# Performance work log

Hardware: AMD Instinct MI355X
Metric: run time of the kernel (lower is better)

## Reference

```python
import jax, jax.numpy as jnp
import numpy as np

D_E = 128
D_R = 128  # must equal D_E for the original torch code to typecheck
BN_EPS = 1e-5


def setup_inputs() -> dict:
    key = jax.random.key(0)
    ks = jax.random.split(key, 8)
    B, S = 16, 2048
    h = jax.random.normal(ks[0], (B, S, D_E), dtype=jnp.float32)
    r = jax.random.normal(ks[1], (B, S, D_R), dtype=jnp.float32)
    t = jax.random.normal(ks[2], (B, S, D_E), dtype=jnp.float32)
    # Xavier-uniform core tensor W: (d_r, d_e, d_e)
    limit = float(np.sqrt(6.0 / (D_R + D_E * D_E)))
    W = jax.random.uniform(ks[3], (D_R, D_E, D_E), minval=-limit, maxval=limit, dtype=jnp.float32)
    # BatchNorm1d params/buffers (inference mode)
    gamma0 = jnp.ones((D_E,), jnp.float32)
    beta0 = jnp.zeros((D_E,), jnp.float32)
    mean0 = 0.1 * jax.random.normal(ks[4], (D_E,), dtype=jnp.float32)
    var0 = jnp.abs(1.0 + 0.1 * jax.random.normal(ks[5], (D_E,), dtype=jnp.float32))
    gamma1 = jnp.ones((D_E,), jnp.float32)
    beta1 = jnp.zeros((D_E,), jnp.float32)
    mean1 = 0.1 * jax.random.normal(ks[6], (D_E,), dtype=jnp.float32)
    var1 = jnp.abs(1.0 + 0.1 * jax.random.normal(ks[7], (D_E,), dtype=jnp.float32))
    return {"h": h, "r": r, "t": t, "W": W,
            "gamma0": gamma0, "beta0": beta0, "mean0": mean0, "var0": var0,
            "gamma1": gamma1, "beta1": beta1, "mean1": mean1, "var1": var1}


def reference(h, r, t, W, gamma0, beta0, mean0, var0, gamma1, beta1, mean1, var1):
    B, S, D = h.shape  # D == d_e == d_r
    N = B * S
    # BatchNorm1d in eval mode over last dim; dropout is identity in eval.
    h_bn = (h - mean0) * jax.lax.rsqrt(var0 + BN_EPS) * gamma0 + beta0
    t_bn = (t - mean1) * jax.lax.rsqrt(var1 + BN_EPS) * gamma1 + beta1
    r2 = r.reshape(N, D)
    # torch.matmul((N,d_r), (d_r,d_e,d_e)) broadcasts -> shape (d_r, N, d_e):
    #   out[k, n, j] = sum_i r2[n, i] * W[k, i, j]
    # followed by .view(N, d_e, d_e) which reinterprets the flat buffer.
    W_mat = jnp.einsum('ni,kij->knj', r2, W).reshape(N, D, D)  # (N, d_e, d_e) after scrambled view
    # hr[n, j] = sum_d h_bn[n, d] * W_mat[n, d, j]
    hr = jnp.einsum('nd,ndj->nj', h_bn.reshape(N, D), W_mat)
    scores = jnp.sum(hr * t_bn.reshape(N, D), axis=-1)  # (N,)
    return scores.reshape(B, S)
```

## Files before the change

kernel.cpp:

```cpp
#include <hip/hip_runtime.h>


typedef __attribute__((ext_vector_type(8))) short bf16x8;
typedef __attribute__((ext_vector_type(4))) short s16x4;
typedef __attribute__((ext_vector_type(4))) float f32x4;

#define DPAD 136
#define BN_EPS 1e-5f

__device__ inline unsigned short f2bf(float f) {
  unsigned u = __builtin_bit_cast(unsigned, f);
  u += 0x7FFFu + ((u >> 16) & 1u);
  return (unsigned short)(u >> 16);
}
__device__ inline float bf2f(unsigned short h) {
  unsigned u = ((unsigned)h) << 16;
  return __builtin_bit_cast(float, u);
}
__device__ inline unsigned pack2bf(float lo, float hi) {
  return (unsigned)f2bf(lo) | ((unsigned)f2bf(hi) << 16);
}
__device__ inline bf16x8 cvt8(f32x4 lo, f32x4 hi) {
  bf16x8 o;
  o[0] = (short)f2bf(lo[0]); o[1] = (short)f2bf(lo[1]);
  o[2] = (short)f2bf(lo[2]); o[3] = (short)f2bf(lo[3]);
  o[4] = (short)f2bf(hi[0]); o[5] = (short)f2bf(hi[1]);
  o[6] = (short)f2bf(hi[2]); o[7] = (short)f2bf(hi[3]);
  return o;
}

__device__ inline int xcd_map(int bid) { return (bid & 7) * 64 + (bid >> 3); }

__global__ __launch_bounds__(256, 3) void k_A(
    const float* __restrict__ t, const float* __restrict__ W,
    const float* __restrict__ gamma1, const float* __restrict__ beta1,
    const float* __restrict__ mean1, const float* __restrict__ var1,
    unsigned short* __restrict__ V) {
  __shared__ short LW[128 * DPAD];
  const int tid = threadIdx.x;
  const int c = tid & 31;
  const int rr = tid >> 5;
  const int wv_ = tid >> 6;
  const int lane = tid & 63;
  const int l16 = lane & 15;
  const int quad = lane >> 4;

  const int wg = xcd_map(blockIdx.x);
  const int k = wg >> 2;
  const int quarter = wg & 3;
  const int nrow = k * 256 + quarter * 64 + wv_ * 16 + l16;

  const float* tp = t + (size_t)nrow * 128;
  bf16x8 tf[4];
#pragma unroll
  for (int ks = 0; ks < 4; ++ks) {
    const int K0 = ks * 32 + quad * 8;
    f32x4 g0 = *(const f32x4*)(gamma1 + K0), g1 = *(const f32x4*)(gamma1 + K0 + 4);
    f32x4 b0 = *(const f32x4*)(beta1  + K0), b1 = *(const f32x4*)(beta1  + K0 + 4);
    f32x4 m0 = *(const f32x4*)(mean1  + K0), m1 = *(const f32x4*)(mean1  + K0 + 4);
    f32x4 v0 = *(const f32x4*)(var1   + K0), v1 = *(const f32x4*)(var1   + K0 + 4);
    f32x4 t0 = *(const f32x4*)(tp + K0),     t1 = *(const f32x4*)(tp + K0 + 4);
    f32x4 lo, hi;
    for (int q = 0; q < 4; ++q) {
      const float s0 = g0[q] * rsqrtf(v0[q] + BN_EPS);
      lo[q] = t0[q] * s0 + (b0[q] - m0[q] * s0);
      const float s1 = g1[q] * rsqrtf(v1[q] + BN_EPS);
      hi[q] = t1[q] * s1 + (b1[q] - m1[q] * s1);
    }
    tf[ks] = cvt8(lo, hi);
  }

  const float* wbase = W + (size_t)k * 16384;
#pragma unroll
  for (int it = 0; it < 16; ++it) {
    const int m = it * 8 + rr;
    f32x4 wvv = *(const f32x4*)(wbase + m * 128 + c * 4);
    s16x4 wb;
    for (int q = 0; q < 4; ++q) wb[q] = (short)f2bf(wvv[q]);
    *(s16x4*)(&LW[m * DPAD + c * 4]) = wb;
  }
  __syncthreads();

  f32x4 acc[8];
#pragma unroll
  for (int nt = 0; nt < 8; ++nt) acc[nt] = (f32x4){0.f, 0.f, 0.f, 0.f};

  __builtin_amdgcn_s_setprio(1);
#pragma unroll
  for (int ks = 0; ks < 4; ++ks) {
    const int K0 = ks * 32 + quad * 8;
    bf16x8 b[8];
#pragma unroll
    for (int nt = 0; nt < 8; ++nt)
      b[nt] = *(const bf16x8*)(&LW[(nt * 16 + l16) * DPAD + K0]);
#pragma unroll
    for (int nt = 0; nt < 8; ++nt)
      acc[nt] = __builtin_amdgcn_mfma_f32_16x16x32_bf16(b[nt], tf[ks], acc[nt], 0, 0, 0);
  }
  __builtin_amdgcn_s_setprio(0);

  const size_t np = (size_t)nrow * 128;
#pragma unroll
  for (int nt = 0; nt < 8; ++nt) {
    unsigned two[2];
    two[0] = pack2bf(acc[nt][0], acc[nt][1]);
    two[1] = pack2bf(acc[nt][2], acc[nt][3]);
    *(uint2*)(V + np + nt * 16 + quad * 4) = *(uint2*)two;
  }
}

__global__ __launch_bounds__(256, 3) void k_B(
    const float* __restrict__ h, const float* __restrict__ r,
    const float* __restrict__ gamma0, const float* __restrict__ beta0,
    const float* __restrict__ mean0, const float* __restrict__ var0,
    const unsigned short* __restrict__ V, float* __restrict__ out) {
  __shared__ short LR[128 * DPAD];
  const int tid = threadIdx.x;
  const int c = tid & 31;
  const int rr = tid >> 5;
  const int wv_ = tid >> 6;
  const int lane = tid & 63;
  const int l16 = lane & 15;
  const int quad = lane >> 4;

  const int wg = xcd_map(blockIdx.x);
  const int low = wg >> 1;
  const int half = wg & 1;
  const int kk = half * 64 + wv_ * 16 + l16;
  const size_t nprow = (size_t)kk * 256 + low;

  const unsigned short* vp = V + nprow * 128;
  bf16x8 vf[4];
#pragma unroll
  for (int ks = 0; ks < 4; ++ks)
    vf[ks] = *(const bf16x8*)(vp + ks * 32 + quad * 8);

  const float* rbase = r + (size_t)low * 16384;
#pragma unroll
  for (int it = 0; it < 16; ++it) {
    const int m = it * 8 + rr;
    f32x4 rv = *(const f32x4*)(rbase + m * 128 + c * 4);
    s16x4 rb;
    for (int q = 0; q < 4; ++q) rb[q] = (short)f2bf(rv[q]);
    *(s16x4*)(&LR[m * DPAD + c * 4]) = rb;
  }
  __syncthreads();

  f32x4 acc[8];
#pragma unroll
  for (int nt = 0; nt < 8; ++nt) acc[nt] = (f32x4){0.f, 0.f, 0.f, 0.f};

  __builtin_amdgcn_s_setprio(1);
#pragma unroll
  for (int ks = 0; ks < 4; ++ks) {
    const int K0 = ks * 32 + quad * 8;
    bf16x8 b[8];
#pragma unroll
    for (int nt = 0; nt < 8; ++nt)
      b[nt] = *(const bf16x8*)(&LR[(nt * 16 + l16) * DPAD + K0]);
#pragma unroll
    for (int nt = 0; nt < 8; ++nt)
      acc[nt] = __builtin_amdgcn_mfma_f32_16x16x32_bf16(b[nt], vf[ks], acc[nt], 0, 0, 0);
  }
  __builtin_amdgcn_s_setprio(0);

  const float* hp = h + nprow * 128;
  float s = 0.f;
#pragma unroll
  for (int nt = 0; nt < 8; ++nt) {
    const int a0 = nt * 16 + quad * 4;
    f32x4 hv = *(const f32x4*)(hp + a0);
    f32x4 g  = *(const f32x4*)(gamma0 + a0);
    f32x4 be = *(const f32x4*)(beta0  + a0);
    f32x4 mu = *(const f32x4*)(mean0  + a0);
    f32x4 va = *(const f32x4*)(var0   + a0);
    for (int q = 0; q < 4; ++q) {
      const float sc = g[q] * rsqrtf(va[q] + BN_EPS);
      const float hb = hv[q] * sc + (be[q] - mu[q] * sc);
      s += hb * acc[nt][q];
    }
  }
  s += __shfl_xor(s, 16, 64);
  s += __shfl_xor(s, 32, 64);
  if (quad == 0) out[nprow] = s;
}

extern "C" void kernel_launch(void* const* d_in, const int* in_sizes, int n_in,
                              void* d_out, int out_size, void* d_ws, size_t ws_size,
                              hipStream_t stream) {
  const float* h      = (const float*)d_in[0];
  const float* r      = (const float*)d_in[1];
  const float* t      = (const float*)d_in[2];
  const float* W      = (const float*)d_in[3];
  const float* gamma0 = (const float*)d_in[4];
  const float* beta0  = (const float*)d_in[5];
  const float* mean0  = (const float*)d_in[6];
  const float* var0   = (const float*)d_in[7];
  const float* gamma1 = (const float*)d_in[8];
  const float* beta1  = (const float*)d_in[9];
  const float* mean1  = (const float*)d_in[10];
  const float* var1   = (const float*)d_in[11];
  float* out = (float*)d_out;

  unsigned short* V = (unsigned short*)d_ws;

  k_A<<<512, 256, 0, stream>>>(t, W, gamma1, beta1, mean1, var1, V);
  k_B<<<512, 256, 0, stream>>>(h, r, gamma0, beta0, mean0, var0, V, out);
}
```

Baseline: 118.5 us.

## Stage W and r tiles into LDS via direct global-to-LDS loads with XOR swizzle

Replaces the register round-trip staging (global load, convert to bf16, LDS store) with global_load_lds direct DMA of fp32 tiles into LDS. An XOR swizzle on 16-byte chunks avoids bank conflicts, and the bf16 conversion moves to fragment read time. The goal is to cut VGPR pressure and staging instructions and to let the loads overlap the t/V fragment loads. The cost is double the LDS footprint (64KB fp32), which lowers occupancy from 3 to 2 blocks, plus redundant conversions, since each fragment element is converted every time it is read.

```diff
diff --git a/kernel.cpp b/kernel.cpp
--- a/kernel.cpp
+++ b/kernel.cpp
@@ -2,20 +2,14 @@
 
 
 typedef __attribute__((ext_vector_type(8))) short bf16x8;
-typedef __attribute__((ext_vector_type(4))) short s16x4;
 typedef __attribute__((ext_vector_type(4))) float f32x4;
 
-#define DPAD 136
 #define BN_EPS 1e-5f
 
 __device__ inline unsigned short f2bf(float f) {
   unsigned u = __builtin_bit_cast(unsigned, f);
   u += 0x7FFFu + ((u >> 16) & 1u);
   return (unsigned short)(u >> 16);
-}
-__device__ inline float bf2f(unsigned short h) {
-  unsigned u = ((unsigned)h) << 16;
-  return __builtin_bit_cast(float, u);
 }
 __device__ inline unsigned pack2bf(float lo, float hi) {
   return (unsigned)f2bf(lo) | ((unsigned)f2bf(hi) << 16);
@@ -29,17 +23,42 @@
   return o;
 }
 
+__device__ inline void gload_lds16(const float* g, void* l) {
+  __builtin_amdgcn_global_load_lds(
+      (const __attribute__((address_space(1))) void*)g,
+      (__attribute__((address_space(3))) void*)l, 16, 0, 0);
+}
+
 __device__ inline int xcd_map(int bid) { return (bid & 7) * 64 + (bid >> 3); }
 
-__global__ __launch_bounds__(256, 3) void k_A(
+__device__ inline void stage_swz(const float* __restrict__ src, float* lds,
+                                 int wv_, int lane) {
+  const int c = lane & 31;
+  const int rw = lane >> 5;
+#pragma unroll
+  for (int it = 0; it < 16; ++it) {
+    const int m0 = it * 8 + wv_ * 2;
+    const int m = m0 + rw;
+    const int gs = c ^ (m & 15);
+    gload_lds16(src + m * 128 + gs * 4, lds + m0 * 128);
+  }
+}
+
+__device__ inline bf16x8 frag_swz(const float* lds, int R, int K0) {
+  const int s0 = K0 >> 2;
+  const int x = R & 15;
+  f32x4 lo = *(const f32x4*)(lds + R * 128 + ((s0 ^ x) << 2));
+  f32x4 hi = *(const f32x4*)(lds + R * 128 + (((s0 + 1) ^ x) << 2));
+  return cvt8(lo, hi);
+}
+
+__global__ __launch_bounds__(256, 2) void k_A(
     const float* __restrict__ t, const float* __restrict__ W,
     const float* __restrict__ gamma1, const float* __restrict__ beta1,
     const float* __restrict__ mean1, const float* __restrict__ var1,
     unsigned short* __restrict__ V) {
-  __shared__ short LW[128 * DPAD];
+  __shared__ float LW[128 * 128];
   const int tid = threadIdx.x;
-  const int c = tid & 31;
-  const int rr = tid >> 5;
   const int wv_ = tid >> 6;
   const int lane = tid & 63;
   const int l16 = lane & 15;
@@ -49,6 +68,8 @@
   const int k = wg >> 2;
   const int quarter = wg & 3;
   const int nrow = k * 256 + quarter * 64 + wv_ * 16 + l16;
+
+  stage_swz(W + (size_t)k * 16384, LW, wv_, lane);
 
   const float* tp = t + (size_t)nrow * 128;
   bf16x8 tf[4];
@@ -69,16 +90,6 @@
     }
     tf[ks] = cvt8(lo, hi);
   }
-
-  const float* wbase = W + (size_t)k * 16384;
-#pragma unroll
-  for (int it = 0; it < 16; ++it) {
-    const int m = it * 8 + rr;
-    f32x4 wvv = *(const f32x4*)(wbase + m * 128 + c * 4);
-    s16x4 wb;
-    for (int q = 0; q < 4; ++q) wb[q] = (short)f2bf(wvv[q]);
-    *(s16x4*)(&LW[m * DPAD + c * 4]) = wb;
-  }
   __syncthreads();
 
   f32x4 acc[8];
@@ -92,7 +103,7 @@
     bf16x8 b[8];
 #pragma unroll
     for (int nt = 0; nt < 8; ++nt)
-      b[nt] = *(const bf16x8*)(&LW[(nt * 16 + l16) * DPAD + K0]);
+      b[nt] = frag_swz(LW, nt * 16 + l16, K0);
 #pragma unroll
     for (int nt = 0; nt < 8; ++nt)
       acc[nt] = __builtin_amdgcn_mfma_f32_16x16x32_bf16(b[nt], tf[ks], acc[nt], 0, 0, 0);
@@ -109,15 +120,13 @@
   }
 }
 
-__global__ __launch_bounds__(256, 3) void k_B(
+__global__ __launch_bounds__(256, 2) void k_B(
     const float* __restrict__ h, const float* __restrict__ r,
     const float* __restrict__ gamma0, const float* __restrict__ beta0,
     const float* __restrict__ mean0, const float* __restrict__ var0,
     const unsigned short* __restrict__ V, float* __restrict__ out) {
-  __shared__ short LR[128 * DPAD];
+  __shared__ float LR[128 * 128];
   const int tid = threadIdx.x;
-  const int c = tid & 31;
-  const int rr = tid >> 5;
   const int wv_ = tid >> 6;
   const int lane = tid & 63;
   const int l16 = lane & 15;
@@ -129,21 +138,13 @@
   const int kk = half * 64 + wv_ * 16 + l16;
   const size_t nprow = (size_t)kk * 256 + low;
 
+  stage_swz(r + (size_t)low * 16384, LR, wv_, lane);
+
   const unsigned short* vp = V + nprow * 128;
   bf16x8 vf[4];
 #pragma unroll
   for (int ks = 0; ks < 4; ++ks)
     vf[ks] = *(const bf16x8*)(vp + ks * 32 + quad * 8);
-
-  const float* rbase = r + (size_t)low * 16384;
-#pragma unroll
-  for (int it = 0; it < 16; ++it) {
-    const int m = it * 8 + rr;
-    f32x4 rv = *(const f32x4*)(rbase + m * 128 + c * 4);
-    s16x4 rb;
-    for (int q = 0; q < 4; ++q) rb[q] = (short)f2bf(rv[q]);
-    *(s16x4*)(&LR[m * DPAD + c * 4]) = rb;
-  }
   __syncthreads();
 
   f32x4 acc[8];
@@ -157,7 +158,7 @@
     bf16x8 b[8];
 #pragma unroll
     for (int nt = 0; nt < 8; ++nt)
-      b[nt] = *(const bf16x8*)(&LR[(nt * 16 + l16) * DPAD + K0]);
+      b[nt] = frag_swz(LR, nt * 16 + l16, K0);
 #pragma unroll
     for (int nt = 0; nt < 8; ++nt)
       acc[nt] = __builtin_amdgcn_mfma_f32_16x16x32_bf16(b[nt], vf[ks], acc[nt], 0, 0, 0);
```

New measurement: 122.2 us. +3.1%, slower.
